# Kernel optimization log

Hardware: AMD Instinct MI355X
Metric: run time of the kernel (lower is better)

## Reference

```python
import jax, jax.numpy as jnp
import numpy as np

N = 50000      # nodes
E = 800000     # edges
CIN = 128
CH = 128
COUT = 64
EPS = 1e-5     # BatchNorm eps


def setup_inputs() -> dict:
    key = jax.random.key(0)
    ks = jax.random.split(key, 16)
    s = 0.1  # weight scale for numerical stability
    return {
        "x": jax.random.normal(ks[0], (N, CIN), jnp.float32),
        "edge_index": jax.random.randint(ks[1], (2, E), 0, N, jnp.int32),
        "edge_weights": jax.random.uniform(ks[2], (E,), jnp.float32),
        "w1": jax.random.normal(ks[3], (CIN, CH), jnp.float32) * s,
        "b1": jnp.zeros((CH,), jnp.float32),
        "bn1_g": jnp.ones((CH,), jnp.float32),
        "bn1_b": jnp.zeros((CH,), jnp.float32),
        "bn1_m": jax.random.normal(ks[4], (CH,), jnp.float32) * 0.1,
        "bn1_v": jax.random.uniform(ks[5], (CH,), jnp.float32) + 0.5,
        "conv_ws": jax.random.normal(ks[6], (2, CH, CH), jnp.float32) * s,
        "conv_bs": jnp.zeros((2, CH), jnp.float32),
        "bns_g": jnp.ones((2, CH), jnp.float32),
        "bns_b": jnp.zeros((2, CH), jnp.float32),
        "bns_m": jax.random.normal(ks[7], (2, CH), jnp.float32) * 0.1,
        "bns_v": jax.random.uniform(ks[8], (2, CH), jnp.float32) + 0.5,
        "lin1_w": jax.random.normal(ks[9], (CH, CH), jnp.float32) * s,
        "lin1_b": jnp.zeros((CH,), jnp.float32),
        "lin2_w": jax.random.normal(ks[10], (CH, COUT), jnp.float32) * s,
        "lin2_b": jnp.zeros((COUT,), jnp.float32),
    }


def _bn(h, g, b, m, v):
    # BatchNorm1d in eval mode: running statistics
    return (h - m) * jax.lax.rsqrt(v + EPS) * g + b


def _gcn(h, w, b, src, dst, norm, n):
    # GCNConv: out[dst] += norm_e * (h @ W)[src]  (self loops already in src/dst)
    h = h @ w
    msg = h[src] * norm[:, None]                 # [E+N, CH]
    return jax.ops.segment_sum(msg, dst, num_segments=n) + b


def reference(x, edge_index, edge_weights, w1, b1, bn1_g, bn1_b, bn1_m, bn1_v,
              conv_ws, conv_bs, bns_g, bns_b, bns_m, bns_v,
              lin1_w, lin1_b, lin2_w, lin2_b):
    n = x.shape[0]
    loop = jnp.arange(n, dtype=edge_index.dtype)
    src = jnp.concatenate([edge_index[0], loop])
    dst = jnp.concatenate([edge_index[1], loop])
    ew = jnp.concatenate([edge_weights, jnp.ones((n,), edge_weights.dtype)])
    # symmetric degree normalization (PyG gcn_norm)
    deg = jax.ops.segment_sum(ew, dst, num_segments=n)
    dis = jnp.where(deg > 0, jax.lax.rsqrt(deg), 0.0)
    norm = dis[src] * ew * dis[dst]

    lrelu = jax.nn.leaky_relu  # slope 0.01, matches F.leaky_relu default
    h = lrelu(_bn(_gcn(x, w1, b1, src, dst, norm, n), bn1_g, bn1_b, bn1_m, bn1_v))
    for i in range(conv_ws.shape[0]):
        h = lrelu(_bn(_gcn(h, conv_ws[i], conv_bs[i], src, dst, norm, n),
                      bns_g[i], bns_b[i], bns_m[i], bns_v[i]) + h)
    h = lrelu(h @ lin1_w + lin1_b)
    # dropout is identity in eval mode
    return h @ lin2_w + lin2_b
```

## Files before the change

### kernel.cpp

```cpp
#include <hip/hip_runtime.h>
#include <hip/hip_bf16.h>


constexpr int   NN    = 50000;
constexpr int   EE    = 800000;
constexpr int   CH    = 128;
constexpr int   SLOTS = 64;
constexpr int   NBUK  = 782;
constexpr int   RCAP  = 2048;
constexpr int   EPB   = 2048;
constexpr int   NB_BIN = (EE + EPB - 1) / EPB;
constexpr int   NB_WZ  = (73728 + 384 + 255) / 256;
constexpr float EPS   = 1e-5f;

typedef __attribute__((ext_vector_type(8))) short bf16x8;
typedef __attribute__((ext_vector_type(4))) float f32x4;
typedef unsigned long long u64;
typedef unsigned short u16;

__device__ inline u16 f2bf_rne(float f) {
  unsigned u = __float_as_uint(f);
  unsigned r = u + 0x7fffu + ((u >> 16) & 1u);
  return (u16)(r >> 16);
}
__device__ inline float bf2f(unsigned h16) {
  return __uint_as_float(h16 << 16);
}


__global__ __launch_bounds__(256) void binw_kernel(
    const int* __restrict__ ei, const float* __restrict__ ew,
    unsigned* __restrict__ gcur, u64* __restrict__ bins,
    const float* __restrict__ w1, const float* __restrict__ bn1_g, const float* __restrict__ bn1_v,
    const float* __restrict__ conv_ws, const float* __restrict__ bns_g, const float* __restrict__ bns_v,
    const float* __restrict__ lin1_w, const float* __restrict__ lin2_w,
    const float* __restrict__ b1, const float* __restrict__ bn1_b, const float* __restrict__ bn1_m,
    const float* __restrict__ conv_bs, const float* __restrict__ bns_b, const float* __restrict__ bns_m,
    u16* __restrict__ w1h, u16* __restrict__ w1l,
    u16* __restrict__ c0h, u16* __restrict__ c0l,
    u16* __restrict__ c1h, u16* __restrict__ c1l,
    u16* __restrict__ l1h, u16* __restrict__ l1l,
    u16* __restrict__ l2h, u16* __restrict__ l2l,
    float* __restrict__ beff)
{
  const int tid = threadIdx.x;
  if (blockIdx.x >= NB_BIN) {
    int idx = (blockIdx.x - NB_BIN) * 256 + tid;
    if (idx >= 73728) {
      int r = idx - 73728;
      if (r >= 384) return;
      int l = r >> 7, c = r & 127;
      float bc, gg, bb, mm, vv;
      if (l == 0) { bc = b1[c]; gg = bn1_g[c]; bb = bn1_b[c]; mm = bn1_m[c]; vv = bn1_v[c]; }
      else {
        int o = (l - 1) * 128 + c;
        bc = conv_bs[o]; gg = bns_g[o]; bb = bns_b[o]; mm = bns_m[o]; vv = bns_v[o];
      }
      beff[r] = (bc - mm) * gg * rsqrtf(vv + EPS) + bb;
      return;
    }
    const float* W; const float* g = nullptr; const float* v = nullptr;
    u16 *hi, *lo; int CO = 128; int local;
    if      (idx < 16384) { W = w1;              g = bn1_g;     v = bn1_v;     hi = w1h; lo = w1l; local = idx; }
    else if (idx < 32768) { W = conv_ws;         g = bns_g;     v = bns_v;     hi = c0h; lo = c0l; local = idx - 16384; }
    else if (idx < 49152) { W = conv_ws + 16384; g = bns_g+128; v = bns_v+128; hi = c1h; lo = c1l; local = idx - 32768; }
    else if (idx < 65536) { W = lin1_w;                                        hi = l1h; lo = l1l; local = idx - 49152; }
    else                  { W = lin2_w;                                        hi = l2h; lo = l2l; local = idx - 65536; CO = 64; }
    int k = local / CO, n = local % CO;
    float w = W[local];
    if (g) w *= g[n] * rsqrtf(v[n] + EPS);
    int NCT = CO / 16;
    int kchunk = k >> 5, kin = k & 31, quad = kin >> 3, j = kin & 7;
    int ct = n >> 4, l = (quad << 4) | (n & 15);
    size_t pos = ((size_t)(kchunk * NCT + ct) * 64 + l) * 8 + j;
    u16 h = f2bf_rne(w);
    hi[pos] = h;
    lo[pos] = f2bf_rne(w - bf2f(h));
    return;
  }
  __shared__ unsigned cnt[NBUK];
  __shared__ unsigned base[NBUK];
  for (int b = tid; b < NBUK; b += 256) cnt[b] = 0;
  __syncthreads();
  const int e0 = blockIdx.x * EPB;
  unsigned pk[8]; u16 bkt[8]; u16 rnk[8]; unsigned char dl[8];
  #pragma unroll
  for (int i = 0; i < 8; i++) {
    int e = e0 + i * 256 + tid;
    if (e < EE) {
      int s = ei[e], d = ei[EE + e];
      float w = ew[e];
      bkt[i] = (u16)(d >> 6);
      dl[i]  = (unsigned char)(d & 63);
      pk[i]  = ((unsigned)f2bf_rne(w) << 16) | (unsigned)s;
      rnk[i] = (u16)atomicAdd(&cnt[bkt[i]], 1u);
    } else bkt[i] = 0xffffu;
  }
  __syncthreads();
  for (int b = tid; b < NBUK; b += 256) {
    unsigned c = cnt[b];
    base[b] = c ? atomicAdd(&gcur[b * 16], c) : 0u;
  }
  __syncthreads();
  #pragma unroll
  for (int i = 0; i < 8; i++) {
    if (bkt[i] == 0xffffu) continue;
    unsigned pos = base[bkt[i]] + rnk[i];
    if (pos < RCAP)
      bins[(size_t)bkt[i] * RCAP + pos] = ((u64)dl[i] << 32) | pk[i];
  }
}


__global__ __launch_bounds__(256) void scatgemm_kernel(
    const unsigned* __restrict__ gcur, const u64* __restrict__ bins,
    unsigned* __restrict__ ell, float* __restrict__ dis,
    const float* __restrict__ Ain,
    const u16* __restrict__ Whi, const u16* __restrict__ Wlo,
    u16* __restrict__ Cout)
{
  __shared__ unsigned rank[64];
  __shared__ float    wsum[64];
  __shared__ float    disl[64];
  __shared__ float    lds[64][CH + 4];
  const int b   = blockIdx.x;
  const int tid = threadIdx.x;

  if (tid < 64) { rank[tid] = 1u; wsum[tid] = 0.f; }
  __syncthreads();
  unsigned cnt = gcur[b * 16];
  if (cnt > RCAP) cnt = RCAP;
  const u64* src = bins + (size_t)b * RCAP;
  for (unsigned i = tid; i < cnt; i += 256) {
    u64 v = src[i];
    unsigned pk = (unsigned)v;
    unsigned dl = (unsigned)(v >> 32);
    unsigned r = atomicAdd(&rank[dl], 1u);
    if (r < SLOTS)
      ell[((size_t)(b * 64 + dl)) * SLOTS + r] = pk;
    atomicAdd(&wsum[dl], bf2f(pk >> 16));
  }
  __syncthreads();
  if (tid < 64) {
    int node = b * 64 + tid;
    float d = rsqrtf(1.0f + wsum[tid]);
    disl[tid] = d;
    if (node < NN) {
      unsigned c = rank[tid];
      if (c > SLOTS) c = SLOTS;
      ell[(size_t)node * SLOTS] = c;
      dis[node] = d;
    }
  }
  __syncthreads();

  const int wave = tid >> 6;
  const int lane = tid & 63;
  const int quad = lane >> 4;
  const int mrow = lane & 15;
  const int row0 = b * 64;

  int arow = row0 + wave * 16 + mrow;
  if (arow >= NN) arow = NN - 1;

  bf16x8 ahi[4], alo[4];
  const float* Ar = Ain + (size_t)arow * CH;
  #pragma unroll
  for (int c = 0; c < 4; c++) {
    int off = c * 32 + quad * 8;
    float4 f0 = *(const float4*)(Ar + off);
    float4 f1 = *(const float4*)(Ar + off + 4);
    float f[8] = {f0.x, f0.y, f0.z, f0.w, f1.x, f1.y, f1.z, f1.w};
    #pragma unroll
    for (int j = 0; j < 8; j++) {
      u16 h = f2bf_rne(f[j]);
      ahi[c][j] = (short)h;
      alo[c][j] = (short)f2bf_rne(f[j] - bf2f(h));
    }
  }

  f32x4 acc[8];
  #pragma unroll
  for (int t = 0; t < 8; t++) acc[t] = (f32x4){0.f, 0.f, 0.f, 0.f};
  #pragma unroll
  for (int c = 0; c < 4; c++) {
    #pragma unroll
    for (int t = 0; t < 8; t++) {
      size_t base = ((size_t)(c * 8 + t) * 64 + lane) * 8;
      bf16x8 bh = *(const bf16x8*)(Whi + base);
      bf16x8 bl = *(const bf16x8*)(Wlo + base);
      acc[t] = __builtin_amdgcn_mfma_f32_16x16x32_bf16(ahi[c], bh, acc[t], 0, 0, 0);
      acc[t] = __builtin_amdgcn_mfma_f32_16x16x32_bf16(alo[c], bh, acc[t], 0, 0, 0);
      acc[t] = __builtin_amdgcn_mfma_f32_16x16x32_bf16(ahi[c], bl, acc[t], 0, 0, 0);
    }
  }

  #pragma unroll
  for (int t = 0; t < 8; t++)
    #pragma unroll
    for (int r = 0; r < 4; r++)
      lds[wave * 16 + quad * 4 + r][t * 16 + mrow] = acc[t][r];
  __syncthreads();

  #pragma unroll
  for (int i = tid; i < 64 * CH / 4; i += 256) {
    int row = (i * 4) / CH;
    int col = (i * 4) % CH;
    int grow = row0 + row;
    if (grow >= NN) continue;
    float rs = disl[row];
    const float* lp = &lds[row][col];
    u16* cp = (u16*)Cout + (size_t)grow * CH + col;
    unsigned p0 = ((unsigned)f2bf_rne(lp[1] * rs) << 16) | f2bf_rne(lp[0] * rs);
    unsigned p1 = ((unsigned)f2bf_rne(lp[3] * rs) << 16) | f2bf_rne(lp[2] * rs);
    *(uint2*)cp = make_uint2(p0, p1);
  }
}

template<bool RES, bool WH>
__device__ __forceinline__ void gather4_qw(
    const u16* __restrict__ hwin, const unsigned* __restrict__ ell,
    const float* __restrict__ dis, const float* __restrict__ beff,
    const u16* __restrict__ res, u16* __restrict__ hout,
    unsigned* __restrict__ hsbase,
    int nbase, int lane, int sub, int grp)
{
  int nd0 = nbase < NN ? nbase : NN - 1;
  unsigned wcur = ell[(size_t)nd0 * SLOTS + lane];
  for (int r = 0; r < 4; r++) {
    int node = nbase + r;
    int nd = node < NN ? node : NN - 1;
    unsigned myword = wcur;
    if (r < 3) {
      int n2 = node + 1 < NN ? node + 1 : NN - 1;
      wcur = ell[(size_t)n2 * SLOTS + lane];
    }
    int cnt = __shfl((int)myword, 0);
    if (cnt > SLOTS) cnt = SLOTS;
    float a[8] = {0.f, 0.f, 0.f, 0.f, 0.f, 0.f, 0.f, 0.f};
    for (int j = 0; j < cnt; j += 16) {
      unsigned sidx[4]; float wv[4];
      #pragma unroll
      for (int q = 0; q < 4; q++) {
        int jj = j + q * 4 + grp;
        unsigned e = (unsigned)__shfl((int)myword, jj & 63);
        float    w = (jj == 0) ? 1.0f : bf2f(e >> 16);
        unsigned s = (jj == 0) ? (unsigned)nd : (e & 0xffffu);
        if (jj >= cnt) { w = 0.f; s = (unsigned)nd; }
        sidx[q] = s; wv[q] = w;
      }
      uint4 h[4];
      #pragma unroll
      for (int q = 0; q < 4; q++)
        h[q] = *(const uint4*)(hwin + (size_t)sidx[q] * CH + sub * 8);
      #pragma unroll
      for (int q = 0; q < 4; q++) {
        float w = wv[q];
        a[0] = fmaf(w, bf2f(h[q].x & 0xffffu), a[0]); a[1] = fmaf(w, bf2f(h[q].x >> 16), a[1]);
        a[2] = fmaf(w, bf2f(h[q].y & 0xffffu), a[2]); a[3] = fmaf(w, bf2f(h[q].y >> 16), a[3]);
        a[4] = fmaf(w, bf2f(h[q].z & 0xffffu), a[4]); a[5] = fmaf(w, bf2f(h[q].z >> 16), a[5]);
        a[6] = fmaf(w, bf2f(h[q].w & 0xffffu), a[6]); a[7] = fmaf(w, bf2f(h[q].w >> 16), a[7]);
      }
    }
    #pragma unroll
    for (int k = 0; k < 8; k++) {
      a[k] += __shfl_xor(a[k], 16);
      a[k] += __shfl_xor(a[k], 32);
    }
    if (grp == 0) {
      float disd = dis[nd];
      int c = sub * 8;
      float4 be0 = *(const float4*)(beff + c);
      float4 be1 = *(const float4*)(beff + c + 4);
      float y[8];
      y[0] = a[0] * disd + be0.x; y[1] = a[1] * disd + be0.y;
      y[2] = a[2] * disd + be0.z; y[3] = a[3] * disd + be0.w;
      y[4] = a[4] * disd + be1.x; y[5] = a[5] * disd + be1.y;
      y[6] = a[6] * disd + be1.z; y[7] = a[7] * disd + be1.w;
      if constexpr (RES) {
        uint4 rr = *(const uint4*)(res + (size_t)nd * CH + c);
        y[0] += bf2f(rr.x & 0xffffu); y[1] += bf2f(rr.x >> 16);
        y[2] += bf2f(rr.y & 0xffffu); y[3] += bf2f(rr.y >> 16);
        y[4] += bf2f(rr.z & 0xffffu); y[5] += bf2f(rr.z >> 16);
        y[6] += bf2f(rr.w & 0xffffu); y[7] += bf2f(rr.w >> 16);
      }
      #pragma unroll
      for (int k = 0; k < 8; k++) y[k] = y[k] > 0.f ? y[k] : 0.01f * y[k];
      uint4 o;
      o.x = ((unsigned)f2bf_rne(y[1]) << 16) | f2bf_rne(y[0]);
      o.y = ((unsigned)f2bf_rne(y[3]) << 16) | f2bf_rne(y[2]);
      o.z = ((unsigned)f2bf_rne(y[5]) << 16) | f2bf_rne(y[4]);
      o.w = ((unsigned)f2bf_rne(y[7]) << 16) | f2bf_rne(y[6]);
      if constexpr (WH) {
        if (node < NN) *(uint4*)(hout + (size_t)node * CH + c) = o;
      }
      *(uint4*)&hsbase[r * 68 + sub * 4] = o;
    }
  }
}

template<bool RES>
__global__ __launch_bounds__(256, 6) void fuse_kernel(
    const u16* __restrict__ hwin,
    const unsigned* __restrict__ ell, const float* __restrict__ dis,
    const float* __restrict__ beff, const u16* __restrict__ res,
    const u16* __restrict__ Whi, const u16* __restrict__ Wlo,
    u16* __restrict__ hout, u16* __restrict__ hwout)
{
  __shared__ unsigned hs[16][68];
  const int tid  = threadIdx.x;
  const int wave = tid >> 6;
  const int lane = tid & 63;
  const int sub  = lane & 15;
  const int grp  = lane >> 4;
  const int row0 = blockIdx.x * 16;

  gather4_qw<RES, true>(hwin, ell, dis, beff, res, hout,
                        &hs[wave * 4][0], row0 + wave * 4, lane, sub, grp);
  __syncthreads();

  bf16x8 af[4];
  #pragma unroll
  for (int c = 0; c < 4; c++)
    af[c] = *(const bf16x8*)&hs[sub][c * 16 + grp * 4];
  __syncthreads();

  f32x4 acc[2];
  #pragma unroll
  for (int t = 0; t < 2; t++) acc[t] = (f32x4){0.f, 0.f, 0.f, 0.f};
  #pragma unroll
  for (int c = 0; c < 4; c++) {
    #pragma unroll
    for (int t = 0; t < 2; t++) {
      size_t base = ((size_t)(c * 8 + wave * 2 + t) * 64 + lane) * 8;
      bf16x8 bh = *(const bf16x8*)(Whi + base);
      bf16x8 bl = *(const bf16x8*)(Wlo + base);
      acc[t] = __builtin_amdgcn_mfma_f32_16x16x32_bf16(af[c], bh, acc[t], 0, 0, 0);
      acc[t] = __builtin_amdgcn_mfma_f32_16x16x32_bf16(af[c], bl, acc[t], 0, 0, 0);
    }
  }

  u16* hs16 = (u16*)&hs[0][0];
  #pragma unroll
  for (int r = 0; r < 4; r++) {
    int row = grp * 4 + r;
    float rs = dis[row0 + row];
    #pragma unroll
    for (int t = 0; t < 2; t++)
      hs16[row * 136 + wave * 32 + t * 16 + sub] = f2bf_rne(acc[t][r] * rs);
  }
  __syncthreads();
  {
    int row   = tid >> 4;
    int chunk = tid & 15;
    uint4 o = *(const uint4*)(hs16 + row * 136 + chunk * 8);
    *(uint4*)(hwout + (size_t)(row0 + row) * CH + chunk * 8) = o;
  }
}

__global__ __launch_bounds__(256, 6) void fuse_last_kernel(
    const u16* __restrict__ hwin,
    const unsigned* __restrict__ ell, const float* __restrict__ dis,
    const float* __restrict__ beff, const u16* __restrict__ res,
    const u16* __restrict__ l1h, const u16* __restrict__ l1l,
    const float* __restrict__ b1,
    const u16* __restrict__ l2h, const u16* __restrict__ l2l,
    const float* __restrict__ b2, float* __restrict__ out)
{
  __shared__ unsigned hs[16][68];
  __shared__ float    fs[16][132];
  const int tid  = threadIdx.x;
  const int wave = tid >> 6;
  const int lane = tid & 63;
  const int sub  = lane & 15;
  const int grp  = lane >> 4;
  const int row0 = blockIdx.x * 16;

  gather4_qw<true, false>(hwin, ell, dis, beff, res, nullptr,
                          &hs[wave * 4][0], row0 + wave * 4, lane, sub, grp);
  __syncthreads();

  bf16x8 af[4];
  #pragma unroll
  for (int c = 0; c < 4; c++)
    af[c] = *(const bf16x8*)&hs[sub][c * 16 + grp * 4];

  f32x4 acc[2];
  #pragma unroll
  for (int t = 0; t < 2; t++) acc[t] = (f32x4){0.f, 0.f, 0.f, 0.f};
  #pragma unroll
  for (int c = 0; c < 4; c++) {
    #pragma unroll
    for (int t = 0; t < 2; t++) {
      size_t base = ((size_t)(c * 8 + wave * 2 + t) * 64 + lane) * 8;
      bf16x8 bh = *(const bf16x8*)(l1h + base);
      bf16x8 bl = *(const bf16x8*)(l1l + base);
      acc[t] = __builtin_amdgcn_mfma_f32_16x16x32_bf16(af[c], bh, acc[t], 0, 0, 0);
      acc[t] = __builtin_amdgcn_mfma_f32_16x16x32_bf16(af[c], bl, acc[t], 0, 0, 0);
    }
  }
  #pragma unroll
  for (int t = 0; t < 2; t++) {
    int col = wave * 32 + t * 16 + sub;
    float bb = b1[col];
    #pragma unroll
    for (int r = 0; r < 4; r++) {
      float x = acc[t][r] + bb;
      x = x > 0.f ? x : 0.01f * x;
      fs[grp * 4 + r][col] = x;
    }
  }
  __syncthreads();

  f32x4 acc2 = (f32x4){0.f, 0.f, 0.f, 0.f};
  #pragma unroll
  for (int c = 0; c < 4; c++) {
    bf16x8 ahi, alo;
    const float* lp = &fs[sub][c * 32 + grp * 8];
    float4 f0 = *(const float4*)lp;
    float4 f1 = *(const float4*)(lp + 4);
    float f[8] = {f0.x, f0.y, f0.z, f0.w, f1.x, f1.y, f1.z, f1.w};
    #pragma unroll
    for (int j = 0; j < 8; j++) {
      u16 h = f2bf_rne(f[j]);
      ahi[j] = (short)h;
      alo[j] = (short)f2bf_rne(f[j] - bf2f(h));
    }
    size_t base = ((size_t)(c * 4 + wave) * 64 + lane) * 8;
    bf16x8 bh = *(const bf16x8*)(l2h + base);
    bf16x8 bl = *(const bf16x8*)(l2l + base);
    acc2 = __builtin_amdgcn_mfma_f32_16x16x32_bf16(ahi, bh, acc2, 0, 0, 0);
    acc2 = __builtin_amdgcn_mfma_f32_16x16x32_bf16(alo, bh, acc2, 0, 0, 0);
    acc2 = __builtin_amdgcn_mfma_f32_16x16x32_bf16(ahi, bl, acc2, 0, 0, 0);
  }
  {
    float bb = b2[wave * 16 + sub];
    #pragma unroll
    for (int r = 0; r < 4; r++) {
      int grow = row0 + grp * 4 + r;
      if (grow < NN)
        out[(size_t)grow * 64 + wave * 16 + sub] = acc2[r] + bb;
    }
  }
}


extern "C" void kernel_launch(void* const* d_in, const int* in_sizes, int n_in,
                              void* d_out, int out_size, void* d_ws, size_t ws_size,
                              hipStream_t stream) {
  const float* x       = (const float*)d_in[0];
  const int*   ei      = (const int*)  d_in[1];
  const float* ew      = (const float*)d_in[2];
  const float* w1      = (const float*)d_in[3];
  const float* b1      = (const float*)d_in[4];
  const float* bn1_g   = (const float*)d_in[5];
  const float* bn1_b   = (const float*)d_in[6];
  const float* bn1_m   = (const float*)d_in[7];
  const float* bn1_v   = (const float*)d_in[8];
  const float* conv_ws = (const float*)d_in[9];
  const float* conv_bs = (const float*)d_in[10];
  const float* bns_g   = (const float*)d_in[11];
  const float* bns_b   = (const float*)d_in[12];
  const float* bns_m   = (const float*)d_in[13];
  const float* bns_v   = (const float*)d_in[14];
  const float* lin1_w  = (const float*)d_in[15];
  const float* lin1_b  = (const float*)d_in[16];
  const float* lin2_w  = (const float*)d_in[17];
  const float* lin2_b  = (const float*)d_in[18];
  float* out = (float*)d_out;

  size_t off = 0;
  auto alloc = [&](size_t elems) -> void* {
    void* p = (char*)d_ws + off * 4;
    off += (elems + 3) & ~(size_t)3;
    return p;
  };
  unsigned* gcur = (unsigned*)alloc(NBUK * 16);
  u64*      bins = (u64*)     alloc((size_t)NBUK * RCAP * 2);
  unsigned* ell  = (unsigned*)alloc((size_t)NN * SLOTS);
  float*    dis  = (float*)   alloc(NN);
  float*    beff = (float*)   alloc(3 * CH);
  u16*      hwa  = (u16*)     alloc((size_t)NN * CH / 2);
  u16*      hwb  = (u16*)     alloc((size_t)NN * CH / 2);
  u16*      h1   = (u16*)     alloc((size_t)NN * CH / 2);
  u16*      h2   = (u16*)     alloc((size_t)NN * CH / 2);
  u16* w1h = (u16*)alloc(CH * CH / 2); u16* w1l = (u16*)alloc(CH * CH / 2);
  u16* c0h = (u16*)alloc(CH * CH / 2); u16* c0l = (u16*)alloc(CH * CH / 2);
  u16* c1h = (u16*)alloc(CH * CH / 2); u16* c1l = (u16*)alloc(CH * CH / 2);
  u16* l1h = (u16*)alloc(CH * CH / 2); u16* l1l = (u16*)alloc(CH * CH / 2);
  u16* l2h = (u16*)alloc(CH * 64 / 2); u16* l2l = (u16*)alloc(CH * 64 / 2);

  const int nb_fuse = (NN + 15) / 16;
  dim3 B(256);

  hipMemsetAsync(gcur, 0, NBUK * 16 * sizeof(unsigned), stream);

  binw_kernel<<<NB_BIN + NB_WZ, B, 0, stream>>>(ei, ew, gcur, bins,
      w1, bn1_g, bn1_v, conv_ws, bns_g, bns_v, lin1_w, lin2_w,
      b1, bn1_b, bn1_m, conv_bs, bns_b, bns_m,
      w1h, w1l, c0h, c0l, c1h, c1l, l1h, l1l, l2h, l2l, beff);

  scatgemm_kernel<<<NBUK, B, 0, stream>>>(gcur, bins, ell, dis, x, w1h, w1l, hwa);

  fuse_kernel<false><<<nb_fuse, B, 0, stream>>>(hwa, ell, dis, beff, nullptr,
      c0h, c0l, h1, hwb);

  fuse_kernel<true><<<nb_fuse, B, 0, stream>>>(hwb, ell, dis, beff + CH, h1,
      c1h, c1l, h2, hwa);

  fuse_last_kernel<<<nb_fuse, B, 0, stream>>>(hwa, ell, dis, beff + 2 * CH, h2,
      l1h, l1l, lin1_b, l2h, l2l, lin2_b, out);
}
```

Baseline: 296.8 us.

## Split scatter and first GEMM into separate blocks, compute degree sums via global atomics

Degree weight sums are now accumulated with global float atomics in the binning kernel instead of shared-memory atomics inside the scatter stage. This lets the scatter kernel launch twice as many blocks: half build the ELL adjacency and the others run the first GEMM independently, reading dis straight from the global sums. Edges per binning block are doubled to halve the block count. In exchange, each edge now issues a global atomic add, and the memset grows to also zero the new degree array, which must sit right after gcur in the workspace.

```diff
diff --git a/kernel.cpp b/kernel.cpp
--- a/kernel.cpp
+++ b/kernel.cpp
@@ -8,7 +8,7 @@
 constexpr int   SLOTS = 64;
 constexpr int   NBUK  = 782;
 constexpr int   RCAP  = 2048;
-constexpr int   EPB   = 2048;
+constexpr int   EPB   = 4096;
 constexpr int   NB_BIN = (EE + EPB - 1) / EPB;
 constexpr int   NB_WZ  = (73728 + 384 + 255) / 256;
 constexpr float EPS   = 1e-5f;
@@ -30,7 +30,7 @@
 
 __global__ __launch_bounds__(256) void binw_kernel(
     const int* __restrict__ ei, const float* __restrict__ ew,
-    unsigned* __restrict__ gcur, u64* __restrict__ bins,
+    unsigned* __restrict__ gcur, u64* __restrict__ bins, float* __restrict__ wsum,
     const float* __restrict__ w1, const float* __restrict__ bn1_g, const float* __restrict__ bn1_v,
     const float* __restrict__ conv_ws, const float* __restrict__ bns_g, const float* __restrict__ bns_v,
     const float* __restrict__ lin1_w, const float* __restrict__ lin2_w,
@@ -83,17 +83,19 @@
   for (int b = tid; b < NBUK; b += 256) cnt[b] = 0;
   __syncthreads();
   const int e0 = blockIdx.x * EPB;
-  unsigned pk[8]; u16 bkt[8]; u16 rnk[8]; unsigned char dl[8];
-  #pragma unroll
-  for (int i = 0; i < 8; i++) {
+  unsigned pk[16]; u16 bkt[16]; u16 rnk[16]; unsigned char dl[16];
+  #pragma unroll
+  for (int i = 0; i < 16; i++) {
     int e = e0 + i * 256 + tid;
     if (e < EE) {
       int s = ei[e], d = ei[EE + e];
       float w = ew[e];
+      u16 wb = f2bf_rne(w);
       bkt[i] = (u16)(d >> 6);
       dl[i]  = (unsigned char)(d & 63);
-      pk[i]  = ((unsigned)f2bf_rne(w) << 16) | (unsigned)s;
+      pk[i]  = ((unsigned)wb << 16) | (unsigned)s;
       rnk[i] = (u16)atomicAdd(&cnt[bkt[i]], 1u);
+      atomicAdd(&wsum[d], bf2f(wb));
     } else bkt[i] = 0xffffu;
   }
   __syncthreads();
@@ -103,7 +105,7 @@
   }
   __syncthreads();
   #pragma unroll
-  for (int i = 0; i < 8; i++) {
+  for (int i = 0; i < 16; i++) {
     if (bkt[i] == 0xffffu) continue;
     unsigned pos = base[bkt[i]] + rnk[i];
     if (pos < RCAP)
@@ -114,51 +116,55 @@
 
 __global__ __launch_bounds__(256) void scatgemm_kernel(
     const unsigned* __restrict__ gcur, const u64* __restrict__ bins,
-    unsigned* __restrict__ ell, float* __restrict__ dis,
+    unsigned* __restrict__ ell, const float* __restrict__ wsum,
+    float* __restrict__ dis,
     const float* __restrict__ Ain,
     const u16* __restrict__ Whi, const u16* __restrict__ Wlo,
     u16* __restrict__ Cout)
 {
   __shared__ unsigned rank[64];
-  __shared__ float    wsum[64];
   __shared__ float    disl[64];
   __shared__ float    lds[64][CH + 4];
-  const int b   = blockIdx.x;
   const int tid = threadIdx.x;
 
-  if (tid < 64) { rank[tid] = 1u; wsum[tid] = 0.f; }
-  __syncthreads();
-  unsigned cnt = gcur[b * 16];
-  if (cnt > RCAP) cnt = RCAP;
-  const u64* src = bins + (size_t)b * RCAP;
-  for (unsigned i = tid; i < cnt; i += 256) {
-    u64 v = src[i];
-    unsigned pk = (unsigned)v;
-    unsigned dl = (unsigned)(v >> 32);
-    unsigned r = atomicAdd(&rank[dl], 1u);
-    if (r < SLOTS)
-      ell[((size_t)(b * 64 + dl)) * SLOTS + r] = pk;
-    atomicAdd(&wsum[dl], bf2f(pk >> 16));
-  }
-  __syncthreads();
-  if (tid < 64) {
-    int node = b * 64 + tid;
-    float d = rsqrtf(1.0f + wsum[tid]);
-    disl[tid] = d;
-    if (node < NN) {
-      unsigned c = rank[tid];
-      if (c > SLOTS) c = SLOTS;
-      ell[(size_t)node * SLOTS] = c;
-      dis[node] = d;
-    }
-  }
-  __syncthreads();
+  if (blockIdx.x < NBUK) {
+    const int b = blockIdx.x;
+    if (tid < 64) rank[tid] = 1u;
+    __syncthreads();
+    unsigned cnt = gcur[b * 16];
+    if (cnt > RCAP) cnt = RCAP;
+    const u64* src = bins + (size_t)b * RCAP;
+    for (unsigned i = tid; i < cnt; i += 256) {
+      u64 v = src[i];
+      unsigned pk = (unsigned)v;
+      unsigned dl = (unsigned)(v >> 32);
+      unsigned r = atomicAdd(&rank[dl], 1u);
+      if (r < SLOTS)
+        ell[((size_t)(b * 64 + dl)) * SLOTS + r] = pk;
+    }
+    __syncthreads();
+    if (tid < 64) {
+      int node = b * 64 + tid;
+      if (node < NN) {
+        unsigned c = rank[tid];
+        if (c > SLOTS) c = SLOTS;
+        ell[(size_t)node * SLOTS] = c;
+        dis[node] = rsqrtf(1.0f + wsum[node]);
+      }
+    }
+    return;
+  }
 
   const int wave = tid >> 6;
   const int lane = tid & 63;
   const int quad = lane >> 4;
   const int mrow = lane & 15;
-  const int row0 = b * 64;
+  const int row0 = (blockIdx.x - NBUK) * 64;
+
+  if (tid < 64) {
+    int node = row0 + tid;
+    disl[tid] = rsqrtf(1.0f + wsum[node < NN ? node : NN - 1]);
+  }
 
   int arow = row0 + wave * 16 + mrow;
   if (arow >= NN) arow = NN - 1;
@@ -476,6 +482,7 @@
     return p;
   };
   unsigned* gcur = (unsigned*)alloc(NBUK * 16);
+  float*    wsum = (float*)   alloc(NN);
   u64*      bins = (u64*)     alloc((size_t)NBUK * RCAP * 2);
   unsigned* ell  = (unsigned*)alloc((size_t)NN * SLOTS);
   float*    dis  = (float*)   alloc(NN);
@@ -493,14 +500,15 @@
   const int nb_fuse = (NN + 15) / 16;
   dim3 B(256);
 
-  hipMemsetAsync(gcur, 0, NBUK * 16 * sizeof(unsigned), stream);
-
-  binw_kernel<<<NB_BIN + NB_WZ, B, 0, stream>>>(ei, ew, gcur, bins,
+  hipMemsetAsync(gcur, 0, (NBUK * 16 + NN) * sizeof(unsigned), stream);
+
+  binw_kernel<<<NB_BIN + NB_WZ, B, 0, stream>>>(ei, ew, gcur, bins, wsum,
       w1, bn1_g, bn1_v, conv_ws, bns_g, bns_v, lin1_w, lin2_w,
       b1, bn1_b, bn1_m, conv_bs, bns_b, bns_m,
       w1h, w1l, c0h, c0l, c1h, c1l, l1h, l1l, l2h, l2l, beff);
 
-  scatgemm_kernel<<<NBUK, B, 0, stream>>>(gcur, bins, ell, dis, x, w1h, w1l, hwa);
+  scatgemm_kernel<<<2 * NBUK, B, 0, stream>>>(gcur, bins, ell, wsum, dis,
+      x, w1h, w1l, hwa);
 
   fuse_kernel<false><<<nb_fuse, B, 0, stream>>>(hwa, ell, dis, beff, nullptr,
       c0h, c0l, h1, hwb);
```

After: 307.3 us. 1.04x slower.
